# Kernel tuning notes

Measured on AMD Instinct MI355X. Metric: run time of the kernel, lower is better.

## Reference

```python
import jax, jax.numpy as jnp
import numpy as np

V, D, H, B, T = 32000, 256, 512, 32, 64


def setup_inputs() -> dict:
    key = jax.random.key(0)
    ks = jax.random.split(key, 8)
    return {
        "word_indices": jax.random.randint(ks[0], (B, T), 0, V),
        "num_words": jax.random.randint(ks[1], (B,), 1, T + 1),
        "encoder_state": jax.random.normal(ks[2], (B, H), jnp.float32),
        # learned params
        "embW": jax.random.uniform(ks[3], (V, D), jnp.float32, -1.0, 1.0),
        "Wg": jax.random.normal(ks[4], (D + H, 2 * H), jnp.float32) * 0.05,  # reset+update gates
        "bg": jnp.ones((2 * H,), jnp.float32),  # TF GRUCell gate bias init = 1.0
        "Wc": jax.random.normal(ks[5], (D + H, H), jnp.float32) * 0.05,      # candidate
        "bc": jnp.zeros((H,), jnp.float32),
        "Wout": jax.random.normal(ks[6], (H, V), jnp.float32) * 0.05,        # Dense(V)
        "bout": jnp.zeros((V,), jnp.float32),
    }


def reference(word_indices, num_words, encoder_state, embW, Wg, bg, Wc, bc, Wout, bout):
    # Embedding lookup: [B, T, D] -> time-major [T, B, D]
    xs = jnp.swapaxes(embW[word_indices], 0, 1)
    # sequence-length mask like tf.nn.static_rnn: [T, B, 1]
    mask = (jnp.arange(T)[:, None] < num_words[None, :])[..., None].astype(xs.dtype)

    def step(h, inp):
        x_t, m_t = inp  # [B, D], [B, 1]
        xh = jnp.concatenate([x_t, h], axis=-1)          # [B, D+H]
        r, u = jnp.split(jax.nn.sigmoid(xh @ Wg + bg), 2, axis=-1)
        c = jnp.tanh(jnp.concatenate([x_t, r * h], axis=-1) @ Wc + bc)
        h_new = u * h + (1.0 - u) * c
        out = h_new * m_t                                 # zero outputs past seq length
        h_next = m_t * h_new + (1.0 - m_t) * h            # carry state past seq length
        return h_next, out

    _, outs = jax.lax.scan(step, encoder_state, (xs, mask))  # outs: [T, B, H]
    logits = jnp.einsum('tbh,hv->btv', outs, Wout) + bout    # [B, T, V]
    return logits
```

## Files before the change

### kernel.cpp

```cpp
#include <hip/hip_runtime.h>
#include <hip/hip_bf16.h>

#define V_ 32000
#define D_ 256
#define H_ 512
#define B_ 32
#define T_ 64
#define NSL 8

typedef __attribute__((ext_vector_type(8))) __bf16 bf16x8;
typedef __attribute__((ext_vector_type(4))) float f32x4;
typedef _Float16 f16x2 __attribute__((ext_vector_type(2)));
typedef unsigned int u32t;
typedef unsigned short u16t;
typedef unsigned long long u64t;

__device__ __forceinline__ u32t pack_h16(float a, float b) {
  union { _Float16 h; unsigned short u; } lo, hi;
  lo.h = (_Float16)a; hi.h = (_Float16)b;
  return (u32t)lo.u | ((u32t)hi.u << 16);
}

__device__ __forceinline__ float f16u_to_f(u16t u) {
  union { _Float16 h; unsigned short u; } x;
  x.u = u;
  return (float)x.h;
}

__device__ __forceinline__ float dot2(u32t w, u32t h, float acc) {
#if __has_builtin(__builtin_amdgcn_fdot2)
  return __builtin_amdgcn_fdot2(__builtin_bit_cast(f16x2, w),
                                __builtin_bit_cast(f16x2, h), acc, false);
#else
  f16x2 a = __builtin_bit_cast(f16x2, w);
  f16x2 b = __builtin_bit_cast(f16x2, h);
  return acc + (float)a.x * (float)b.x + (float)a.y * (float)b.y;
#endif
}

__device__ __forceinline__ void gld_lds16(const void* g, void* l) {
  __builtin_amdgcn_global_load_lds((const __attribute__((address_space(1))) void*)g,
                                   (__attribute__((address_space(3))) void*)l,
                                   16, 0, 0);
}

__device__ __forceinline__ u32t ld_rlx(const u32t* p) {
  return __hip_atomic_load(p, __ATOMIC_RELAXED, __HIP_MEMORY_SCOPE_AGENT);
}
__device__ __forceinline__ void st_rlx(u32t* p, u32t v) {
  __hip_atomic_store(p, v, __ATOMIC_RELAXED, __HIP_MEMORY_SCOPE_AGENT);
}

__global__ __launch_bounds__(256) void k_transpose(const float* __restrict__ Wout,
                                                   __hip_bfloat16* __restrict__ WoutT) {
  __shared__ float tile[64][65];
  int v0 = blockIdx.x * 64;
  int h0 = blockIdx.y * 64;
  int tid = threadIdx.x;
#pragma unroll
  for (int i = 0; i < 16; ++i) {
    int idx = i * 256 + tid;
    int r = idx >> 6;
    int c = idx & 63;
    tile[r][c] = Wout[(size_t)(h0 + r) * V_ + v0 + c];
  }
  __syncthreads();
#pragma unroll
  for (int i = 0; i < 16; ++i) {
    int idx = i * 256 + tid;
    int rv = idx >> 6;
    int ch = idx & 63;
    WoutT[(size_t)(v0 + rv) * H_ + h0 + ch] = __float2bfloat16(tile[ch][rv]);
  }
}

__global__ __launch_bounds__(256) void k_pack_g2(const float* __restrict__ Wg,
                                                 uint4* __restrict__ Wg2) {
  int gid = blockIdx.x * 256 + threadIdx.x;
  int ks = gid & 3;
  int cq = (gid >> 2) & 127;
  int it = (gid >> 9) & 15;
  int s = gid >> 13;
  int j = (cq < 64) ? (s * 64 + cq) : (512 + s * 64 + (cq - 64));
  int k0 = ks * 128 + it * 8;
  uint4 v;
  v.x = pack_h16(Wg[(size_t)(256 + k0 + 0) * 1024 + j], Wg[(size_t)(256 + k0 + 1) * 1024 + j]);
  v.y = pack_h16(Wg[(size_t)(256 + k0 + 2) * 1024 + j], Wg[(size_t)(256 + k0 + 3) * 1024 + j]);
  v.z = pack_h16(Wg[(size_t)(256 + k0 + 4) * 1024 + j], Wg[(size_t)(256 + k0 + 5) * 1024 + j]);
  v.w = pack_h16(Wg[(size_t)(256 + k0 + 6) * 1024 + j], Wg[(size_t)(256 + k0 + 7) * 1024 + j]);
  Wg2[gid] = v;
}
__global__ __launch_bounds__(256) void k_pack_c2(const float* __restrict__ Wc,
                                                 uint4* __restrict__ Wc2) {
  int gid = blockIdx.x * 256 + threadIdx.x;
  int ks8 = gid & 7;
  int cq2 = (gid >> 3) & 63;
  int it = (gid >> 9) & 7;
  int s = gid >> 12;
  int jc = s * 64 + cq2;
  int k0 = ks8 * 64 + it * 8;
  uint4 v;
  v.x = pack_h16(Wc[(size_t)(256 + k0 + 0) * 512 + jc], Wc[(size_t)(256 + k0 + 1) * 512 + jc]);
  v.y = pack_h16(Wc[(size_t)(256 + k0 + 2) * 512 + jc], Wc[(size_t)(256 + k0 + 3) * 512 + jc]);
  v.z = pack_h16(Wc[(size_t)(256 + k0 + 4) * 512 + jc], Wc[(size_t)(256 + k0 + 5) * 512 + jc]);
  v.w = pack_h16(Wc[(size_t)(256 + k0 + 6) * 512 + jc], Wc[(size_t)(256 + k0 + 7) * 512 + jc]);
  Wc2[gid] = v;
}

__global__ __launch_bounds__(256) void k_precompute_g(const int* __restrict__ widx,
                                                      const float* __restrict__ embW,
                                                      const float* __restrict__ Wg,
                                                      const float* __restrict__ bg,
                                                      float* __restrict__ pre_g) {
  __shared__ __align__(16) float x2[D_][8];
  __shared__ int wid[8];
  int tid = threadIdx.x;
  int n0 = blockIdx.x * 8;
  if (tid < 8) wid[tid] = widx[n0 + tid];
  __syncthreads();
#pragma unroll
  for (int i = 0; i < 8; ++i)
    x2[tid][i] = embW[(size_t)wid[i] * D_ + tid];
  __syncthreads();

  int J = blockIdx.y * 256 + tid;
  float bias = bg[J];
  float acc[8];
#pragma unroll
  for (int i = 0; i < 8; ++i) acc[i] = bias;
  for (int d = 0; d < D_; ++d) {
    float4 xa = *(const float4*)&x2[d][0];
    float4 xb = *(const float4*)&x2[d][4];
    float w = Wg[(size_t)d * 1024 + J];
    acc[0] = fmaf(xa.x, w, acc[0]); acc[1] = fmaf(xa.y, w, acc[1]);
    acc[2] = fmaf(xa.z, w, acc[2]); acc[3] = fmaf(xa.w, w, acc[3]);
    acc[4] = fmaf(xb.x, w, acc[4]); acc[5] = fmaf(xb.y, w, acc[5]);
    acc[6] = fmaf(xb.z, w, acc[6]); acc[7] = fmaf(xb.w, w, acc[7]);
  }
#pragma unroll
  for (int i = 0; i < 8; ++i)
    pre_g[(size_t)(n0 + i) * 1024 + J] = acc[i];
}

__global__ __launch_bounds__(256) void k_precompute_c(const int* __restrict__ widx,
                                                      const float* __restrict__ embW,
                                                      const float* __restrict__ Wc,
                                                      const float* __restrict__ bc,
                                                      float* __restrict__ pre_c) {
  __shared__ __align__(16) float x2[D_][8];
  __shared__ int wid[8];
  int tid = threadIdx.x;
  int n0 = blockIdx.x * 8;
  if (tid < 8) wid[tid] = widx[n0 + tid];
  __syncthreads();
#pragma unroll
  for (int i = 0; i < 8; ++i)
    x2[tid][i] = embW[(size_t)wid[i] * D_ + tid];
  __syncthreads();

  int Jc = blockIdx.y * 256 + tid;
  float bias = bc[Jc];
  float acc[8];
#pragma unroll
  for (int i = 0; i < 8; ++i) acc[i] = bias;
  for (int d = 0; d < D_; ++d) {
    float4 xa = *(const float4*)&x2[d][0];
    float4 xb = *(const float4*)&x2[d][4];
    float w = Wc[(size_t)d * 512 + Jc];
    acc[0] = fmaf(xa.x, w, acc[0]); acc[1] = fmaf(xa.y, w, acc[1]);
    acc[2] = fmaf(xa.z, w, acc[2]); acc[3] = fmaf(xa.w, w, acc[3]);
    acc[4] = fmaf(xb.x, w, acc[4]); acc[5] = fmaf(xb.y, w, acc[5]);
    acc[6] = fmaf(xb.z, w, acc[6]); acc[7] = fmaf(xb.w, w, acc[7]);
  }
#pragma unroll
  for (int i = 0; i < 8; ++i)
    pre_c[(size_t)(n0 + i) * 512 + Jc] = acc[i];
}

__global__ __launch_bounds__(256) void k_gru_init(const float* __restrict__ enc,
                                                  u32t* __restrict__ HBT,
                                                  u32t* __restrict__ RHT) {
  int gid = blockIdx.x * 256 + threadIdx.x;
  int b = gid >> 9, k = gid & 511;
  u32t hv = pack_h16(enc[b * H_ + k], 0.f) & 0xffffu;
  st_rlx(&HBT[gid], hv);
  st_rlx(&RHT[gid], 0xFFFF0000u);
}

__global__ __launch_bounds__(512, 2) void k_gru7(const int* __restrict__ num_words,
                                                 const uint4* __restrict__ Wg2,
                                                 const uint4* __restrict__ Wc2,
                                                 const float* __restrict__ pre_g,
                                                 const float* __restrict__ pre_c,
                                                 u32t* __restrict__ RHT,
                                                 u32t* __restrict__ HBT,
                                                 u32t* __restrict__ A32) {
  __shared__ __align__(16) u32t h2_l[256];
  __shared__ __align__(16) u32t rh2_l[256];
  __shared__ float u_l[64];
  int bid = blockIdx.x;
  int b = bid & 31;
  int s = bid >> 5;
  int tid = threadIdx.x;
  int nw = num_words[b];

  int cq = tid >> 2, ks = tid & 3;
  int j1 = (cq < 64) ? (s * 64 + cq) : (512 + s * 64 + (cq - 64));
  int cq2 = tid >> 3, ks8 = tid & 7;
  int jc = s * 64 + cq2;

  uint4 wg[16];
#pragma unroll
  for (int i = 0; i < 16; ++i) {
    int ii = (i + ks) & 15;
    wg[i] = Wg2[(((size_t)s * 16 + ii) * 128 + cq) * 4 + ks];
  }
  uint4 wc[8];
#pragma unroll
  for (int i = 0; i < 8; ++i) {
    int ii = (i + ks8) & 7;
    wc[i] = Wc2[(((size_t)s * 8 + ii) * 64 + cq2) * 8 + ks8];
  }

  u32t* HBp = HBT + (size_t)b * 512;
  u32t* RHp = RHT + (size_t)b * 512;
  bool pub1 = (ks == 0) && (cq < 64);
  bool ulane = (ks == 0) && (cq >= 64);
  bool pub2 = (ks8 == 0);
  bool writer2 = pub2 && ((cq2 & 1) == 0);

  for (int t = 0; t < T_; ++t) {
    float pg = pre_g[((size_t)b * T_ + t) * 1024 + j1];
    float pc = pre_c[((size_t)b * T_ + t) * 512 + jc];

    __syncthreads();
    {
      u32t want = (u32t)t << 16;
      u32t v;
      do { v = ld_rlx(&HBp[tid]); } while ((v & 0xffff0000u) != want);
      ((volatile u16t*)h2_l)[tid] = (u16t)v;
    }
    __syncthreads();

    float a = 0.f;
    const uint4* h4 = (const uint4*)h2_l;
#pragma unroll
    for (int i = 0; i < 16; ++i) {
      int ii = (i + ks) & 15;
      uint4 hv = h4[ks * 16 + ii];
      a = dot2(wg[i].x, hv.x, a);
      a = dot2(wg[i].y, hv.y, a);
      a = dot2(wg[i].z, hv.z, a);
      a = dot2(wg[i].w, hv.w, a);
    }
    a += __shfl_xor(a, 1);
    a += __shfl_xor(a, 2);
    float gate = 1.f / (1.f + __expf(-(a + pg)));
    if (cq < 64) {
      float hh = f16u_to_f(((const u16t*)h2_l)[s * 64 + cq]);
      if (pub1)
        st_rlx(&RHp[s * 64 + cq],
               (pack_h16(gate * hh, 0.f) & 0xffffu) | ((u32t)(t + 1) << 16));
    } else if (ulane) {
      u_l[cq - 64] = gate;
    }

    {
      u32t want = (u32t)(t + 1) << 16;
      u32t v;
      do { v = ld_rlx(&RHp[tid]); } while ((v & 0xffff0000u) != want);
      ((volatile u16t*)rh2_l)[tid] = (u16t)v;
    }
    __syncthreads();

    float a2 = 0.f;
    const uint4* r4 = (const uint4*)rh2_l;
#pragma unroll
    for (int i = 0; i < 8; ++i) {
      int ii = (i + ks8) & 7;
      uint4 rv = r4[ks8 * 8 + ii];
      a2 = dot2(wc[i].x, rv.x, a2);
      a2 = dot2(wc[i].y, rv.y, a2);
      a2 = dot2(wc[i].z, rv.z, a2);
      a2 = dot2(wc[i].w, rv.w, a2);
    }
    a2 += __shfl_xor(a2, 1);
    a2 += __shfl_xor(a2, 2);
    a2 += __shfl_xor(a2, 4);
    float cv = tanhf(a2 + pc);
    float uu = u_l[cq2];
    float hold = f16u_to_f(((const u16t*)h2_l)[jc]);
    float hn = uu * hold + (1.f - uu) * cv;
    bool live = t < nw;
    float hnext = live ? hn : hold;
    if (pub2)
      st_rlx(&HBp[s * 64 + cq2],
             (pack_h16(hnext, 0.f) & 0xffffu) | ((u32t)(t + 1) << 16));
    u32t ma = (u32t)__hip_bfloat16_raw(__float2bfloat16(live ? hn : 0.f)).x;
    u32t oa = (u32t)__shfl_xor((int)ma, 8);
    if (writer2)
      A32[(((size_t)b * T_ + t) * 512 + jc) >> 1] = ma | (oa << 16);
  }
}

__global__ __launch_bounds__(256) void k_proj(const __hip_bfloat16* __restrict__ Ap,
                                              const __hip_bfloat16* __restrict__ BTp,
                                              const float* __restrict__ bout,
                                              float* __restrict__ C) {
  __shared__ char As[128 * 64 * 2];
  __shared__ char Bs[128 * 64 * 2];
  int tid = threadIdx.x;
  int lane = tid & 63;
  int wave = tid >> 6;
  int m0 = blockIdx.x * 128;
  int n0 = blockIdx.y * 128;
  int wm = wave >> 1, wn = wave & 1;
  f32x4 acc[4][4] = {};

  const char* Ab = (const char*)Ap;
  const char* Bb = (const char*)BTp;

  for (int ks = 0; ks < 8; ++ks) {
    int k0 = ks * 64;
    __syncthreads();
#pragma unroll
    for (int inst = 0; inst < 4; ++inst) {
      int o = inst * 4096 + wave * 1024;
      int ol = o + lane * 16;
      int r = ol >> 7;
      int cb = ol & 127;
      gld_lds16(Ab + ((size_t)(m0 + r) * 512 + k0) * 2 + cb, As + o);
      gld_lds16(Bb + ((size_t)(n0 + r) * 512 + k0) * 2 + cb, Bs + o);
    }
    __syncthreads();
#pragma unroll
    for (int kk = 0; kk < 64; kk += 32) {
      bf16x8 af[4], bfr[4];
      int cbyte = kk * 2 + ((lane >> 4) << 4);
#pragma unroll
      for (int mi = 0; mi < 4; ++mi) {
        int row = wm * 64 + mi * 16 + (lane & 15);
        af[mi] = *(const bf16x8*)(As + row * 128 + cbyte);
      }
#pragma unroll
      for (int ni = 0; ni < 4; ++ni) {
        int row = wn * 64 + ni * 16 + (lane & 15);
        bfr[ni] = *(const bf16x8*)(Bs + row * 128 + cbyte);
      }
#pragma unroll
      for (int mi = 0; mi < 4; ++mi)
#pragma unroll
        for (int ni = 0; ni < 4; ++ni)
          acc[mi][ni] = __builtin_amdgcn_mfma_f32_16x16x32_bf16(af[mi], bfr[ni], acc[mi][ni], 0, 0, 0);
    }
  }
#pragma unroll
  for (int ni = 0; ni < 4; ++ni) {
    int col = n0 + wn * 64 + ni * 16 + (lane & 15);
    float bb = bout[col];
#pragma unroll
    for (int mi = 0; mi < 4; ++mi) {
      int rbase = m0 + wm * 64 + mi * 16 + ((lane >> 4) << 2);
#pragma unroll
      for (int rr = 0; rr < 4; ++rr) {
        C[(size_t)(rbase + rr) * V_ + col] = acc[mi][ni][rr] + bb;
      }
    }
  }
}

extern "C" void kernel_launch(void* const* d_in, const int* in_sizes, int n_in,
                              void* d_out, int out_size, void* d_ws, size_t ws_size,
                              hipStream_t stream) {
  const int* widx = (const int*)d_in[0];
  const int* num_words = (const int*)d_in[1];
  const float* enc = (const float*)d_in[2];
  const float* embW = (const float*)d_in[3];
  const float* Wg = (const float*)d_in[4];
  const float* bg = (const float*)d_in[5];
  const float* Wc = (const float*)d_in[6];
  const float* bc = (const float*)d_in[7];
  const float* Wout = (const float*)d_in[8];
  const float* bout = (const float*)d_in[9];
  float* out = (float*)d_out;

  char* ws = (char*)d_ws;
  float* pre_g = (float*)(ws);
  float* pre_c = (float*)(ws + 8388608);
  __hip_bfloat16* A = (__hip_bfloat16*)(ws + 12582912);
  __hip_bfloat16* WoutT = (__hip_bfloat16*)(ws + 14680064);
  uint4* Wg2 = (uint4*)(ws + 47448064);
  uint4* Wc2 = (uint4*)(ws + 48496640);
  u32t* RHT = (u32t*)(ws + 49020928);
  u32t* HBT = (u32t*)(ws + 49086464);

  hipLaunchKernelGGL(k_pack_g2, dim3(256), dim3(256), 0, stream, Wg, Wg2);
  hipLaunchKernelGGL(k_pack_c2, dim3(128), dim3(256), 0, stream, Wc, Wc2);
  hipLaunchKernelGGL(k_transpose, dim3(500, 8), dim3(256), 0, stream, Wout, WoutT);
  hipLaunchKernelGGL(k_precompute_g, dim3(256, 4), dim3(256), 0, stream,
                     widx, embW, Wg, bg, pre_g);
  hipLaunchKernelGGL(k_precompute_c, dim3(256, 2), dim3(256), 0, stream,
                     widx, embW, Wc, bc, pre_c);
  hipLaunchKernelGGL(k_gru_init, dim3(64), dim3(256), 0, stream, enc, HBT, RHT);
  hipLaunchKernelGGL(k_gru7, dim3(32 * NSL), dim3(512), 0, stream,
                     num_words, Wg2, Wc2, pre_g, pre_c, RHT, HBT, (u32t*)A);
  hipLaunchKernelGGL(k_proj, dim3(16, 250), dim3(256), 0, stream, A, WoutT, bout, out);
}
```

Before: 390.5 us.

## Merge prep kernels, split GRU dot accumulators, vectorize projection output stores

Three small prep kernels (gate and candidate weight packing plus state init) are merged into one launch, and the two precompute kernels into one grid, cutting launch count and gaps between kernels. The GRU recurrent dot products now use four independent accumulators to shorten the serial dependency chain on each step. The projection GEMM swaps MFMA operands so each lane holds four consecutive output columns, allowing float4 bias loads and float4 stores to the large logits output. These are independent tweaks across several kernels; the float accumulation order changes slightly in the GRU.

```diff
diff --git a/kernel.cpp b/kernel.cpp
--- a/kernel.cpp
+++ b/kernel.cpp
@@ -74,44 +74,60 @@
   }
 }
 
-__global__ __launch_bounds__(256) void k_pack_g2(const float* __restrict__ Wg,
-                                                 uint4* __restrict__ Wg2) {
-  int gid = blockIdx.x * 256 + threadIdx.x;
-  int ks = gid & 3;
-  int cq = (gid >> 2) & 127;
-  int it = (gid >> 9) & 15;
-  int s = gid >> 13;
-  int j = (cq < 64) ? (s * 64 + cq) : (512 + s * 64 + (cq - 64));
-  int k0 = ks * 128 + it * 8;
-  uint4 v;
-  v.x = pack_h16(Wg[(size_t)(256 + k0 + 0) * 1024 + j], Wg[(size_t)(256 + k0 + 1) * 1024 + j]);
-  v.y = pack_h16(Wg[(size_t)(256 + k0 + 2) * 1024 + j], Wg[(size_t)(256 + k0 + 3) * 1024 + j]);
-  v.z = pack_h16(Wg[(size_t)(256 + k0 + 4) * 1024 + j], Wg[(size_t)(256 + k0 + 5) * 1024 + j]);
-  v.w = pack_h16(Wg[(size_t)(256 + k0 + 6) * 1024 + j], Wg[(size_t)(256 + k0 + 7) * 1024 + j]);
-  Wg2[gid] = v;
-}
-__global__ __launch_bounds__(256) void k_pack_c2(const float* __restrict__ Wc,
-                                                 uint4* __restrict__ Wc2) {
-  int gid = blockIdx.x * 256 + threadIdx.x;
-  int ks8 = gid & 7;
-  int cq2 = (gid >> 3) & 63;
-  int it = (gid >> 9) & 7;
-  int s = gid >> 12;
-  int jc = s * 64 + cq2;
-  int k0 = ks8 * 64 + it * 8;
-  uint4 v;
-  v.x = pack_h16(Wc[(size_t)(256 + k0 + 0) * 512 + jc], Wc[(size_t)(256 + k0 + 1) * 512 + jc]);
-  v.y = pack_h16(Wc[(size_t)(256 + k0 + 2) * 512 + jc], Wc[(size_t)(256 + k0 + 3) * 512 + jc]);
-  v.z = pack_h16(Wc[(size_t)(256 + k0 + 4) * 512 + jc], Wc[(size_t)(256 + k0 + 5) * 512 + jc]);
-  v.w = pack_h16(Wc[(size_t)(256 + k0 + 6) * 512 + jc], Wc[(size_t)(256 + k0 + 7) * 512 + jc]);
-  Wc2[gid] = v;
-}
-
-__global__ __launch_bounds__(256) void k_precompute_g(const int* __restrict__ widx,
-                                                      const float* __restrict__ embW,
-                                                      const float* __restrict__ Wg,
-                                                      const float* __restrict__ bg,
-                                                      float* __restrict__ pre_g) {
+__global__ __launch_bounds__(256) void k_prep(const float* __restrict__ Wg,
+                                              const float* __restrict__ Wc,
+                                              const float* __restrict__ enc,
+                                              uint4* __restrict__ Wg2,
+                                              uint4* __restrict__ Wc2,
+                                              u32t* __restrict__ HBT,
+                                              u32t* __restrict__ RHT) {
+  int blk = blockIdx.x;
+  int tid = threadIdx.x;
+  if (blk < 256) {
+    int gid = blk * 256 + tid;
+    int ks = gid & 3;
+    int cq = (gid >> 2) & 127;
+    int it = (gid >> 9) & 15;
+    int s = gid >> 13;
+    int j = (cq < 64) ? (s * 64 + cq) : (512 + s * 64 + (cq - 64));
+    int k0 = ks * 128 + it * 8;
+    uint4 v;
+    v.x = pack_h16(Wg[(size_t)(256 + k0 + 0) * 1024 + j], Wg[(size_t)(256 + k0 + 1) * 1024 + j]);
+    v.y = pack_h16(Wg[(size_t)(256 + k0 + 2) * 1024 + j], Wg[(size_t)(256 + k0 + 3) * 1024 + j]);
+    v.z = pack_h16(Wg[(size_t)(256 + k0 + 4) * 1024 + j], Wg[(size_t)(256 + k0 + 5) * 1024 + j]);
+    v.w = pack_h16(Wg[(size_t)(256 + k0 + 6) * 1024 + j], Wg[(size_t)(256 + k0 + 7) * 1024 + j]);
+    Wg2[gid] = v;
+  } else if (blk < 384) {
+    int gid = (blk - 256) * 256 + tid;
+    int ks8 = gid & 7;
+    int cq2 = (gid >> 3) & 63;
+    int it = (gid >> 9) & 7;
+    int s = gid >> 12;
+    int jc = s * 64 + cq2;
+    int k0 = ks8 * 64 + it * 8;
+    uint4 v;
+    v.x = pack_h16(Wc[(size_t)(256 + k0 + 0) * 512 + jc], Wc[(size_t)(256 + k0 + 1) * 512 + jc]);
+    v.y = pack_h16(Wc[(size_t)(256 + k0 + 2) * 512 + jc], Wc[(size_t)(256 + k0 + 3) * 512 + jc]);
+    v.z = pack_h16(Wc[(size_t)(256 + k0 + 4) * 512 + jc], Wc[(size_t)(256 + k0 + 5) * 512 + jc]);
+    v.w = pack_h16(Wc[(size_t)(256 + k0 + 6) * 512 + jc], Wc[(size_t)(256 + k0 + 7) * 512 + jc]);
+    Wc2[gid] = v;
+  } else {
+    int gid = (blk - 384) * 256 + tid;
+    int b = gid >> 9, k = gid & 511;
+    u32t hv = pack_h16(enc[b * H_ + k], 0.f) & 0xffffu;
+    st_rlx(&HBT[gid], hv);
+    st_rlx(&RHT[gid], 0xFFFF0000u);
+  }
+}
+
+__global__ __launch_bounds__(256) void k_precompute(const int* __restrict__ widx,
+                                                    const float* __restrict__ embW,
+                                                    const float* __restrict__ Wg,
+                                                    const float* __restrict__ bg,
+                                                    const float* __restrict__ Wc,
+                                                    const float* __restrict__ bc,
+                                                    float* __restrict__ pre_g,
+                                                    float* __restrict__ pre_c) {
   __shared__ __align__(16) float x2[D_][8];
   __shared__ int wid[8];
   int tid = threadIdx.x;
@@ -123,68 +139,42 @@
     x2[tid][i] = embW[(size_t)wid[i] * D_ + tid];
   __syncthreads();
 
-  int J = blockIdx.y * 256 + tid;
-  float bias = bg[J];
   float acc[8];
-#pragma unroll
-  for (int i = 0; i < 8; ++i) acc[i] = bias;
-  for (int d = 0; d < D_; ++d) {
-    float4 xa = *(const float4*)&x2[d][0];
-    float4 xb = *(const float4*)&x2[d][4];
-    float w = Wg[(size_t)d * 1024 + J];
-    acc[0] = fmaf(xa.x, w, acc[0]); acc[1] = fmaf(xa.y, w, acc[1]);
-    acc[2] = fmaf(xa.z, w, acc[2]); acc[3] = fmaf(xa.w, w, acc[3]);
-    acc[4] = fmaf(xb.x, w, acc[4]); acc[5] = fmaf(xb.y, w, acc[5]);
-    acc[6] = fmaf(xb.z, w, acc[6]); acc[7] = fmaf(xb.w, w, acc[7]);
-  }
-#pragma unroll
-  for (int i = 0; i < 8; ++i)
-    pre_g[(size_t)(n0 + i) * 1024 + J] = acc[i];
-}
-
-__global__ __launch_bounds__(256) void k_precompute_c(const int* __restrict__ widx,
-                                                      const float* __restrict__ embW,
-                                                      const float* __restrict__ Wc,
-                                                      const float* __restrict__ bc,
-                                                      float* __restrict__ pre_c) {
-  __shared__ __align__(16) float x2[D_][8];
-  __shared__ int wid[8];
-  int tid = threadIdx.x;
-  int n0 = blockIdx.x * 8;
-  if (tid < 8) wid[tid] = widx[n0 + tid];
-  __syncthreads();
-#pragma unroll
-  for (int i = 0; i < 8; ++i)
-    x2[tid][i] = embW[(size_t)wid[i] * D_ + tid];
-  __syncthreads();
-
-  int Jc = blockIdx.y * 256 + tid;
-  float bias = bc[Jc];
-  float acc[8];
-#pragma unroll
-  for (int i = 0; i < 8; ++i) acc[i] = bias;
-  for (int d = 0; d < D_; ++d) {
-    float4 xa = *(const float4*)&x2[d][0];
-    float4 xb = *(const float4*)&x2[d][4];
-    float w = Wc[(size_t)d * 512 + Jc];
-    acc[0] = fmaf(xa.x, w, acc[0]); acc[1] = fmaf(xa.y, w, acc[1]);
-    acc[2] = fmaf(xa.z, w, acc[2]); acc[3] = fmaf(xa.w, w, acc[3]);
-    acc[4] = fmaf(xb.x, w, acc[4]); acc[5] = fmaf(xb.y, w, acc[5]);
-    acc[6] = fmaf(xb.z, w, acc[6]); acc[7] = fmaf(xb.w, w, acc[7]);
-  }
-#pragma unroll
-  for (int i = 0; i < 8; ++i)
-    pre_c[(size_t)(n0 + i) * 512 + Jc] = acc[i];
-}
-
-__global__ __launch_bounds__(256) void k_gru_init(const float* __restrict__ enc,
-                                                  u32t* __restrict__ HBT,
-                                                  u32t* __restrict__ RHT) {
-  int gid = blockIdx.x * 256 + threadIdx.x;
-  int b = gid >> 9, k = gid & 511;
-  u32t hv = pack_h16(enc[b * H_ + k], 0.f) & 0xffffu;
-  st_rlx(&HBT[gid], hv);
-  st_rlx(&RHT[gid], 0xFFFF0000u);
+  if (blockIdx.y < 4) {
+    int J = blockIdx.y * 256 + tid;
+    float bias = bg[J];
+#pragma unroll
+    for (int i = 0; i < 8; ++i) acc[i] = bias;
+    for (int d = 0; d < D_; ++d) {
+      float4 xa = *(const float4*)&x2[d][0];
+      float4 xb = *(const float4*)&x2[d][4];
+      float w = Wg[(size_t)d * 1024 + J];
+      acc[0] = fmaf(xa.x, w, acc[0]); acc[1] = fmaf(xa.y, w, acc[1]);
+      acc[2] = fmaf(xa.z, w, acc[2]); acc[3] = fmaf(xa.w, w, acc[3]);
+      acc[4] = fmaf(xb.x, w, acc[4]); acc[5] = fmaf(xb.y, w, acc[5]);
+      acc[6] = fmaf(xb.z, w, acc[6]); acc[7] = fmaf(xb.w, w, acc[7]);
+    }
+#pragma unroll
+    for (int i = 0; i < 8; ++i)
+      pre_g[(size_t)(n0 + i) * 1024 + J] = acc[i];
+  } else {
+    int Jc = (blockIdx.y - 4) * 256 + tid;
+    float bias = bc[Jc];
+#pragma unroll
+    for (int i = 0; i < 8; ++i) acc[i] = bias;
+    for (int d = 0; d < D_; ++d) {
+      float4 xa = *(const float4*)&x2[d][0];
+      float4 xb = *(const float4*)&x2[d][4];
+      float w = Wc[(size_t)d * 512 + Jc];
+      acc[0] = fmaf(xa.x, w, acc[0]); acc[1] = fmaf(xa.y, w, acc[1]);
+      acc[2] = fmaf(xa.z, w, acc[2]); acc[3] = fmaf(xa.w, w, acc[3]);
+      acc[4] = fmaf(xb.x, w, acc[4]); acc[5] = fmaf(xb.y, w, acc[5]);
+      acc[6] = fmaf(xb.z, w, acc[6]); acc[7] = fmaf(xb.w, w, acc[7]);
+    }
+#pragma unroll
+    for (int i = 0; i < 8; ++i)
+      pre_c[(size_t)(n0 + i) * 512 + Jc] = acc[i];
+  }
 }
 
 __global__ __launch_bounds__(512, 2) void k_gru7(const int* __restrict__ num_words,
@@ -242,17 +232,18 @@
     }
     __syncthreads();
 
-    float a = 0.f;
+    float a0 = 0.f, a1 = 0.f, a2s = 0.f, a3 = 0.f;
     const uint4* h4 = (const uint4*)h2_l;
 #pragma unroll
     for (int i = 0; i < 16; ++i) {
       int ii = (i + ks) & 15;
       uint4 hv = h4[ks * 16 + ii];
-      a = dot2(wg[i].x, hv.x, a);
-      a = dot2(wg[i].y, hv.y, a);
-      a = dot2(wg[i].z, hv.z, a);
-      a = dot2(wg[i].w, hv.w, a);
-    }
+      a0 = dot2(wg[i].x, hv.x, a0);
+      a1 = dot2(wg[i].y, hv.y, a1);
+      a2s = dot2(wg[i].z, hv.z, a2s);
+      a3 = dot2(wg[i].w, hv.w, a3);
+    }
+    float a = (a0 + a1) + (a2s + a3);
     a += __shfl_xor(a, 1);
     a += __shfl_xor(a, 2);
     float gate = 1.f / (1.f + __expf(-(a + pg)));
@@ -273,17 +264,18 @@
     }
     __syncthreads();
 
-    float a2 = 0.f;
+    float c0 = 0.f, c1 = 0.f, c2 = 0.f, c3 = 0.f;
     const uint4* r4 = (const uint4*)rh2_l;
 #pragma unroll
     for (int i = 0; i < 8; ++i) {
       int ii = (i + ks8) & 7;
       uint4 rv = r4[ks8 * 8 + ii];
-      a2 = dot2(wc[i].x, rv.x, a2);
-      a2 = dot2(wc[i].y, rv.y, a2);
-      a2 = dot2(wc[i].z, rv.z, a2);
-      a2 = dot2(wc[i].w, rv.w, a2);
-    }
+      c0 = dot2(wc[i].x, rv.x, c0);
+      c1 = dot2(wc[i].y, rv.y, c1);
+      c2 = dot2(wc[i].z, rv.z, c2);
+      c3 = dot2(wc[i].w, rv.w, c3);
+    }
+    float a2 = (c0 + c1) + (c2 + c3);
     a2 += __shfl_xor(a2, 1);
     a2 += __shfl_xor(a2, 2);
     a2 += __shfl_xor(a2, 4);
@@ -351,20 +343,22 @@
       for (int mi = 0; mi < 4; ++mi)
 #pragma unroll
         for (int ni = 0; ni < 4; ++ni)
-          acc[mi][ni] = __builtin_amdgcn_mfma_f32_16x16x32_bf16(af[mi], bfr[ni], acc[mi][ni], 0, 0, 0);
+          acc[mi][ni] = __builtin_amdgcn_mfma_f32_16x16x32_bf16(bfr[ni], af[mi], acc[mi][ni], 0, 0, 0);
     }
   }
 #pragma unroll
   for (int ni = 0; ni < 4; ++ni) {
-    int col = n0 + wn * 64 + ni * 16 + (lane & 15);
-    float bb = bout[col];
+    int colbase = n0 + wn * 64 + ni * 16 + ((lane >> 4) << 2);
+    float4 bb = *(const float4*)&bout[colbase];
 #pragma unroll
     for (int mi = 0; mi < 4; ++mi) {
-      int rbase = m0 + wm * 64 + mi * 16 + ((lane >> 4) << 2);
-#pragma unroll
-      for (int rr = 0; rr < 4; ++rr) {
-        C[(size_t)(rbase + rr) * V_ + col] = acc[mi][ni][rr] + bb;
-      }
+      int row = m0 + wm * 64 + mi * 16 + (lane & 15);
+      float4 v;
+      v.x = acc[mi][ni][0] + bb.x;
+      v.y = acc[mi][ni][1] + bb.y;
+      v.z = acc[mi][ni][2] + bb.z;
+      v.w = acc[mi][ni][3] + bb.w;
+      *(float4*)&C[(size_t)row * V_ + colbase] = v;
     }
   }
 }
@@ -394,14 +388,11 @@
   u32t* RHT = (u32t*)(ws + 49020928);
   u32t* HBT = (u32t*)(ws + 49086464);
 
-  hipLaunchKernelGGL(k_pack_g2, dim3(256), dim3(256), 0, stream, Wg, Wg2);
-  hipLaunchKernelGGL(k_pack_c2, dim3(128), dim3(256), 0, stream, Wc, Wc2);
+  hipLaunchKernelGGL(k_prep, dim3(448), dim3(256), 0, stream,
+                     Wg, Wc, enc, Wg2, Wc2, HBT, RHT);
   hipLaunchKernelGGL(k_transpose, dim3(500, 8), dim3(256), 0, stream, Wout, WoutT);
-  hipLaunchKernelGGL(k_precompute_g, dim3(256, 4), dim3(256), 0, stream,
-                     widx, embW, Wg, bg, pre_g);
-  hipLaunchKernelGGL(k_precompute_c, dim3(256, 2), dim3(256), 0, stream,
-                     widx, embW, Wc, bc, pre_c);
-  hipLaunchKernelGGL(k_gru_init, dim3(64), dim3(256), 0, stream, enc, HBT, RHT);
+  hipLaunchKernelGGL(k_precompute, dim3(256, 6), dim3(256), 0, stream,
+                     widx, embW, Wg, bg, Wc, bc, pre_g, pre_c);
   hipLaunchKernelGGL(k_gru7, dim3(32 * NSL), dim3(512), 0, stream,
                      num_words, Wg2, Wc2, pre_g, pre_c, RHT, HBT, (u32t*)A);
   hipLaunchKernelGGL(k_proj, dim3(16, 250), dim3(256), 0, stream, A, WoutT, bout, out);
```

Result: no change. 392.3 us (+0.5%).
